# Optimization experiments

Hardware: AMD Instinct MI355X
Metric: run time of the kernel (lower is better)

The kernel has to match this reference:

```python
import math
import jax, jax.numpy as jnp
import numpy as np

H = 2048
T = 8192
NUM_LAYERS = 24
LAYER_ID = 6


def setup_inputs() -> dict:
    key = jax.random.key(0)
    ks = jax.random.split(key, 5)
    ratio_0_to_1 = LAYER_ID / (NUM_LAYERS - 1)
    ratio_1_to_almost_0 = 1.0 - LAYER_ID / NUM_LAYERS
    # parameter init exactly as in RwkvSelfAttention.__init__
    zigzag = 0.5 * (jnp.arange(1, H + 1) % 3 - 1)
    time_first = jnp.full((H,), math.log(0.3), jnp.float32) + zigzag.astype(jnp.float32)
    hh = jnp.arange(0, H, dtype=jnp.float32)
    time_decay = -5.0 + 8.0 * (hh / (H - 1)) ** (0.7 + 1.3 * ratio_0_to_1)
    xx = jnp.arange(H, dtype=jnp.float32) / H
    time_mix_key = jnp.power(xx, ratio_1_to_almost_0)
    time_mix_value = time_mix_key + 0.3 * ratio_0_to_1
    time_mix_receptance = jnp.power(xx, 0.5 * ratio_1_to_almost_0)
    scale = 1.0 / math.sqrt(H)
    return {
        "hidden": jax.random.normal(ks[0], (T, H), jnp.float32),
        "sx": jnp.zeros((H,), jnp.float32),
        "aa": jnp.zeros((H,), jnp.float32),
        "bb": jnp.zeros((H,), jnp.float32),
        "pp": jnp.full((H,), -1e30, jnp.float32),  # log-space -inf init
        "time_decay": time_decay,
        "time_first": time_first,
        "time_mix_key": time_mix_key,
        "time_mix_value": time_mix_value,
        "time_mix_receptance": time_mix_receptance,
        "Wk": jax.random.normal(ks[1], (H, H), jnp.float32) * scale,
        "Wv": jax.random.normal(ks[2], (H, H), jnp.float32) * scale,
        "Wr": jax.random.normal(ks[3], (H, H), jnp.float32) * scale,
        "Wo": jax.random.normal(ks[4], (H, H), jnp.float32) * scale,
    }


def reference(hidden, sx, aa, bb, pp, time_decay, time_first, time_mix_key,
              time_mix_value, time_mix_receptance, Wk, Wv, Wr, Wo):
    # token-shift mix: c_x[t] = hidden[t-1], c_x[0] = sx
    c_x = jnp.concatenate((sx[None, :], hidden[:-1, :]), axis=0)  # [T, H]
    key_x = hidden * time_mix_key + c_x * (1.0 - time_mix_key)
    value_x = hidden * time_mix_value + c_x * (1.0 - time_mix_value)
    receptance_x = hidden * time_mix_receptance + c_x * (1.0 - time_mix_receptance)

    r = jax.nn.sigmoid(receptance_x @ Wr)  # [T, H]
    k = key_x @ Wk                         # [T, H]
    v = value_x @ Wv                       # [T, H]

    w_decay = -jnp.exp(time_decay)  # [H]

    def step(state, kv):
        a, b, p = state
        kk, vv = kv
        # output with bonus (time_first)
        ww = time_first + kk
        q = jnp.maximum(p, ww)
        e1 = jnp.exp(p - q)
        e2 = jnp.exp(ww - q)
        out_t = (e1 * a + e2 * vv) / (e1 * b + e2)
        # state update with decay
        ww2 = w_decay + p
        q2 = jnp.maximum(ww2, kk)
        e1b = jnp.exp(ww2 - q2)
        e2b = jnp.exp(kk - q2)
        return (e1b * a + e2b * vv, e1b * b + e2b, q2), out_t

    (aa, bb, pp), wkv = jax.lax.scan(step, (aa, bb, pp), (k, v))  # wkv: [T, H]

    out = hidden + (r * wkv) @ Wo
    return out, hidden[-1, :], aa, bb, pp
```

## Files before the change

kernel.cpp:

```cpp
#include <hip/hip_runtime.h>
#include <stdint.h>

#define H 2048
#define T 8192
#define C_CH 128
#define L_CH 64

typedef unsigned short u16;
typedef unsigned int u32;

__device__ __forceinline__ float bf2f(u16 u) {
  return __uint_as_float(((u32)u) << 16);
}
__device__ __forceinline__ u16 f2bf(float f) {
  u32 u = __float_as_uint(f);
  u = u + 0x7FFFu + ((u >> 16) & 1u);
  return (u16)(u >> 16);
}
__device__ __forceinline__ bool in_is_bf16(const u32* ppw) {
  u32 w = ppw[0];
  return (w >> 16) == (w & 0xFFFFu);
}
__device__ __forceinline__ float ldin(const void* p, size_t i, bool bf) {
  return bf ? bf2f(((const u16*)p)[i]) : ((const float*)p)[i];
}
__device__ __forceinline__ void stout(void* p, size_t i, float v, bool bf) {
  if (bf) ((u16*)p)[i] = f2bf(v);
  else ((float*)p)[i] = v;
}

__global__ void mix3_kernel(const void* __restrict__ hidden,
                            const void* __restrict__ sx,
                            const void* __restrict__ tmk,
                            const void* __restrict__ tmv,
                            const void* __restrict__ tmr,
                            u16* __restrict__ outk, u16* __restrict__ outv,
                            u16* __restrict__ outr, const u32* __restrict__ ppw) {
  bool bf = in_is_bf16(ppw);
  int i = blockIdx.x * blockDim.x + threadIdx.x;
  int h = i & (H - 1);
  float hv = ldin(hidden, (size_t)i, bf);
  float cv = (i < H) ? ldin(sx, (size_t)h, bf) : ldin(hidden, (size_t)i - H, bf);
  float d = hv - cv;
  outk[i] = f2bf(cv + ldin(tmk, (size_t)h, bf) * d);
  outv[i] = f2bf(cv + ldin(tmv, (size_t)h, bf) * d);
  outr[i] = f2bf(cv + ldin(tmr, (size_t)h, bf) * d);
}

__global__ void transpose_kernel(const void* __restrict__ W, u16* __restrict__ Wt,
                                 const u32* __restrict__ ppw) {
  bool bf = in_is_bf16(ppw);
  __shared__ u16 tile[32][33];
  int bx = blockIdx.x * 32, by = blockIdx.y * 32;
  int tx = threadIdx.x, ty = threadIdx.y;
#pragma unroll
  for (int j = 0; j < 32; j += 8)
    tile[ty + j][tx] = f2bf(ldin(W, (size_t)(by + ty + j) * H + bx + tx, bf));
  __syncthreads();
#pragma unroll
  for (int j = 0; j < 32; j += 8)
    Wt[(size_t)(bx + ty + j) * H + by + tx] = tile[tx][ty + j];
}

typedef short bf16x8 __attribute__((ext_vector_type(8)));
typedef float f32x4 __attribute__((ext_vector_type(4)));

#define MODE_K 0
#define MODE_BF16 1
#define MODE_SIG 2
#define MODE_ADDH 3

__device__ __forceinline__ void gl_lds16(const short* g, short* l) {
  __builtin_amdgcn_global_load_lds((__attribute__((address_space(1))) void*)(g),
                                   (__attribute__((address_space(3))) void*)(l),
                                   16, 0, 0);
}

template <int MODE>
__global__ __launch_bounds__(256) void gemm_kernel(
    const u16* __restrict__ Au, const u16* __restrict__ Btu,
    void* __restrict__ C, const void* __restrict__ hid,
    const u32* __restrict__ ppw) {
  __shared__ short As[128 * 64];
  __shared__ short Bs[128 * 64];
  const short* A = (const short*)Au;
  const short* Bt = (const short*)Btu;

  const int bid = blockIdx.x;
  const int xcd = bid & 7;
  const int s = bid >> 3;
  const int mblk = (xcd << 3) | (s & 7);
  const int nblk = s >> 3;
  const int m0 = mblk * 128;
  const int n0 = nblk * 128;

  const int tid = threadIdx.x;
  const int lane = tid & 63;
  const int wid = tid >> 6;
  const int wm = wid >> 1;
  const int wn = wid & 1;
  const int lrow = lane & 15;
  const int quad = lane >> 4;

  const int srow = lane >> 2;
  const int scol = (lane & 3) * 8;
  const short* gA = A + (size_t)(m0 + wid * 32 + srow) * H + scol;
  const short* gB = Bt + (size_t)(n0 + wid * 32 + srow) * H + scol;
  short* lA = As + wid * 1024;
  short* lB = Bs + wid * 1024;

  f32x4 acc[4][4];
#pragma unroll
  for (int i = 0; i < 4; i++)
#pragma unroll
    for (int j = 0; j < 4; j++) acc[i][j] = (f32x4){0.f, 0.f, 0.f, 0.f};

  for (int k0 = 0; k0 < H; k0 += 64) {
    __syncthreads();
    gl_lds16(gA + k0, lA);
    gl_lds16(gA + k0 + 16 * H, lA + 512);
    gl_lds16(gB + k0, lB);
    gl_lds16(gB + k0 + 16 * H, lB + 512);
    gl_lds16(gA + k0 + 32, lA + 4096);
    gl_lds16(gA + k0 + 32 + 16 * H, lA + 4096 + 512);
    gl_lds16(gB + k0 + 32, lB + 4096);
    gl_lds16(gB + k0 + 32 + 16 * H, lB + 4096 + 512);
    __syncthreads();
#pragma unroll
    for (int sub = 0; sub < 2; sub++) {
      const short* as = As + sub * 4096;
      const short* bs = Bs + sub * 4096;
      bf16x8 af[4], bfr[4];
#pragma unroll
      for (int i = 0; i < 4; i++)
        af[i] = *(const bf16x8*)(as + (wm * 64 + i * 16 + lrow) * 32 + quad * 8);
#pragma unroll
      for (int j = 0; j < 4; j++)
        bfr[j] = *(const bf16x8*)(bs + (wn * 64 + j * 16 + lrow) * 32 + quad * 8);
#pragma unroll
      for (int i = 0; i < 4; i++)
#pragma unroll
        for (int j = 0; j < 4; j++)
          acc[i][j] = __builtin_amdgcn_mfma_f32_16x16x32_bf16(af[i], bfr[j], acc[i][j], 0, 0, 0);
    }
  }

  bool bf = (MODE == MODE_ADDH) ? in_is_bf16(ppw) : true;
#pragma unroll
  for (int i = 0; i < 4; i++) {
#pragma unroll
    for (int j = 0; j < 4; j++) {
#pragma unroll
      for (int reg = 0; reg < 4; reg++) {
        int row = m0 + wm * 64 + i * 16 + quad * 4 + reg;
        int col = n0 + wn * 64 + j * 16 + lrow;
        size_t idx = (size_t)row * H + col;
        float val = acc[i][j][reg];
        if (MODE == MODE_K || MODE == MODE_BF16) {
          ((u16*)C)[idx] = f2bf(val);
        } else if (MODE == MODE_SIG) {
          ((u16*)C)[idx] = f2bf(1.0f / (1.0f + __expf(-val)));
        } else {
          stout(C, idx, val + ldin(hid, idx, bf), bf);
        }
      }
    }
  }
}

__global__ __launch_bounds__(256) void wkv_local_kernel(
    const u16* __restrict__ kbuf, const u16* __restrict__ vbuf,
    const void* __restrict__ tdec,
    float* __restrict__ suma, float* __restrict__ sumb, float* __restrict__ sump,
    const u32* __restrict__ ppw) {
  bool bf = in_is_bf16(ppw);
  int h = blockIdx.x * 256 + threadIdx.x;
  int c = blockIdx.y;
  float w = -__expf(ldin(tdec, h, bf));
  float a = 0.f, b = 0.f, p = -1e30f;
  size_t base = (size_t)c * L_CH * H + h;
#pragma unroll 4
  for (int t = 0; t < L_CH; t++) {
    size_t idx = base + (size_t)t * H;
    float kk = bf2f(kbuf[idx]);
    float vv = bf2f(vbuf[idx]);
    float ww2 = w + p;
    float q2 = fmaxf(ww2, kk);
    float e1b = __expf(ww2 - q2), e2b = __expf(kk - q2);
    a = e1b * a + e2b * vv;
    b = e1b * b + e2b;
    p = q2;
  }
  suma[(size_t)c * H + h] = a;
  sumb[(size_t)c * H + h] = b;
  sump[(size_t)c * H + h] = p;
}

__global__ __launch_bounds__(256) void wkv_prefix_kernel(
    const float* __restrict__ suma, const float* __restrict__ sumb,
    const float* __restrict__ sump,
    const void* __restrict__ aa_in, const void* __restrict__ bb_in,
    const void* __restrict__ pp_in, const void* __restrict__ tdec,
    const void* __restrict__ hidden,
    float* __restrict__ sta, float* __restrict__ stb, float* __restrict__ stp,
    void* __restrict__ dout, const u32* __restrict__ ppw) {
  bool bf = in_is_bf16(ppw);
  int h = blockIdx.x * 256 + threadIdx.x;
  float a = ldin(aa_in, h, bf), b = ldin(bb_in, h, bf), p = ldin(pp_in, h, bf);
  float w = -__expf(ldin(tdec, h, bf));
  float wL = w * (float)L_CH;
  for (int c = 0; c < C_CH; c++) {
    size_t i = (size_t)c * H + h;
    sta[i] = a;
    stb[i] = b;
    stp[i] = p;
    float la = suma[i], lb = sumb[i], lp = sump[i];
    float pd = p + wL;
    float q = fmaxf(pd, lp);
    float e1 = __expf(pd - q), e2 = __expf(lp - q);
    a = e1 * a + e2 * la;
    b = e1 * b + e2 * lb;
    p = q;
  }
  size_t base = (size_t)T * H;
  stout(dout, base + h, ldin(hidden, (size_t)(T - 1) * H + h, bf), bf);
  stout(dout, base + H + h, a, bf);
  stout(dout, base + 2 * H + h, b, bf);
  stout(dout, base + 3 * H + h, p, bf);
}

__global__ __launch_bounds__(256) void wkv_out_kernel(
    const u16* __restrict__ kbuf, const u16* __restrict__ vbuf,
    const u16* __restrict__ rbuf,
    const float* __restrict__ sta, const float* __restrict__ stb,
    const float* __restrict__ stp,
    const void* __restrict__ tdec, const void* __restrict__ tfirst,
    u16* __restrict__ rw, const u32* __restrict__ ppw) {
  bool bf = in_is_bf16(ppw);
  int h = blockIdx.x * 256 + threadIdx.x;
  int c = blockIdx.y;
  size_t si = (size_t)c * H + h;
  float a = sta[si], b = stb[si], p = stp[si];
  float tf = ldin(tfirst, h, bf);
  float w = -__expf(ldin(tdec, h, bf));
  size_t base = (size_t)c * L_CH * H + h;
#pragma unroll 4
  for (int t = 0; t < L_CH; t++) {
    size_t idx = base + (size_t)t * H;
    float kk = bf2f(kbuf[idx]);
    float vv = bf2f(vbuf[idx]);
    float rr = bf2f(rbuf[idx]);
    float ww = tf + kk;
    float q = fmaxf(p, ww);
    float e1 = __expf(p - q), e2 = __expf(ww - q);
    float wkv = (e1 * a + e2 * vv) / (e1 * b + e2);
    rw[idx] = f2bf(rr * wkv);
    float ww2 = w + p;
    float q2 = fmaxf(ww2, kk);
    float e1b = __expf(ww2 - q2), e2b = __expf(kk - q2);
    a = e1b * a + e2b * vv;
    b = e1b * b + e2b;
    p = q2;
  }
}

extern "C" void kernel_launch(void* const* d_in, const int* in_sizes, int n_in,
                              void* d_out, int out_size, void* d_ws, size_t ws_size,
                              hipStream_t stream) {
  const void* hidden = d_in[0];
  const void* sx = d_in[1];
  const void* aa = d_in[2];
  const void* bb = d_in[3];
  const void* pp = d_in[4];
  const void* tdec = d_in[5];
  const void* tfirst = d_in[6];
  const void* tmk = d_in[7];
  const void* tmv = d_in[8];
  const void* tmr = d_in[9];
  const void* Wk = d_in[10];
  const void* Wv = d_in[11];
  const void* Wr = d_in[12];
  const void* Wo = d_in[13];
  const u32* ppw = (const u32*)d_in[4];

  char* ws = (char*)d_ws;
  const size_t TH2 = (size_t)T * H * 2;
  const size_t WT2 = (size_t)H * H * 2;
  u16* A1 = (u16*)ws;
  u16* A2 = (u16*)(ws + TH2);
  u16* A3 = (u16*)(ws + 2 * TH2);
  u16* B1 = (u16*)(ws + 3 * TH2);
  u16* Wt_buf = (u16*)(ws + 4 * TH2);
  float* suma = (float*)(ws + 4 * TH2 + WT2);
  float* sumb = suma + (size_t)C_CH * H;
  float* sump = sumb + (size_t)C_CH * H;
  float* sta = sump + (size_t)C_CH * H;
  float* stb = sta + (size_t)C_CH * H;
  float* stp = stb + (size_t)C_CH * H;

  dim3 mixG((T * H) / 256), mixB(256);
  dim3 trG(64, 64), trB(32, 8);
  dim3 gG(1024), gB(256);
  dim3 scG(H / 256, C_CH), scB(256);

  mix3_kernel<<<mixG, mixB, 0, stream>>>(hidden, sx, tmk, tmv, tmr,
                                         A1, A2, A3, ppw);
  transpose_kernel<<<trG, trB, 0, stream>>>(Wr, Wt_buf, ppw);
  gemm_kernel<MODE_SIG><<<gG, gB, 0, stream>>>(A3, Wt_buf, B1, nullptr, ppw);
  transpose_kernel<<<trG, trB, 0, stream>>>(Wk, Wt_buf, ppw);
  gemm_kernel<MODE_K><<<gG, gB, 0, stream>>>(A1, Wt_buf, A3, nullptr, ppw);
  transpose_kernel<<<trG, trB, 0, stream>>>(Wv, Wt_buf, ppw);
  gemm_kernel<MODE_BF16><<<gG, gB, 0, stream>>>(A2, Wt_buf, A1, nullptr, ppw);
  wkv_local_kernel<<<scG, scB, 0, stream>>>(A3, A1, tdec, suma, sumb, sump, ppw);
  wkv_prefix_kernel<<<dim3(H / 256), scB, 0, stream>>>(
      suma, sumb, sump, aa, bb, pp, tdec, hidden, sta, stb, stp, d_out, ppw);
  wkv_out_kernel<<<scG, scB, 0, stream>>>(A3, A1, B1, sta, stb, stp,
                                          tdec, tfirst, A2, ppw);
  transpose_kernel<<<trG, trB, 0, stream>>>(Wo, Wt_buf, ppw);
  gemm_kernel<MODE_ADDH><<<gG, gB, 0, stream>>>(A2, Wt_buf, d_out, hidden, ppw);
}
```

Baseline: 672.1 us.

## Double-buffer LDS tiles in bf16 GEMM to overlap global loads with MFMA

Splits the LDS tile into two 32-wide K buffers and stages the next half-tile with global_load_lds while MFMAs run on the current one. The aim is to hide global-memory latency that the old load-all, sync, compute loop left exposed. Total LDS use stays the same, but each barrier now covers half as much K. The overlap only happens if the compiler's vmcnt waits do not force the in-flight prefetch to finish before the current buffer is read.

```diff
diff --git a/kernel.cpp b/kernel.cpp
--- a/kernel.cpp
+++ b/kernel.cpp
@@ -81,8 +81,8 @@
     const u16* __restrict__ Au, const u16* __restrict__ Btu,
     void* __restrict__ C, const void* __restrict__ hid,
     const u32* __restrict__ ppw) {
-  __shared__ short As[128 * 64];
-  __shared__ short Bs[128 * 64];
+  __shared__ short As[2][128 * 32];
+  __shared__ short Bs[2][128 * 32];
   const short* A = (const short*)Au;
   const short* Bt = (const short*)Btu;
 
@@ -106,8 +106,7 @@
   const int scol = (lane & 3) * 8;
   const short* gA = A + (size_t)(m0 + wid * 32 + srow) * H + scol;
   const short* gB = Bt + (size_t)(n0 + wid * 32 + srow) * H + scol;
-  short* lA = As + wid * 1024;
-  short* lB = Bs + wid * 1024;
+  const int lofs = wid * 1024;
 
   f32x4 acc[4][4];
 #pragma unroll
@@ -115,35 +114,40 @@
 #pragma unroll
     for (int j = 0; j < 4; j++) acc[i][j] = (f32x4){0.f, 0.f, 0.f, 0.f};
 
+#define STAGE(kk, buf)                                   \
+  do {                                                   \
+    gl_lds16(gA + (kk), &As[buf][lofs]);                 \
+    gl_lds16(gA + (kk) + 16 * H, &As[buf][lofs + 512]);  \
+    gl_lds16(gB + (kk), &Bs[buf][lofs]);                 \
+    gl_lds16(gB + (kk) + 16 * H, &Bs[buf][lofs + 512]);  \
+  } while (0)
+
+#define COMPUTE(buf)                                                          \
+  do {                                                                        \
+    bf16x8 af[4], bfr[4];                                                     \
+    _Pragma("unroll") for (int i = 0; i < 4; i++)                             \
+        af[i] = *(const bf16x8*)(&As[buf][(wm * 64 + i * 16 + lrow) * 32 +    \
+                                          quad * 8]);                         \
+    _Pragma("unroll") for (int j = 0; j < 4; j++)                             \
+        bfr[j] = *(const bf16x8*)(&Bs[buf][(wn * 64 + j * 16 + lrow) * 32 +   \
+                                           quad * 8]);                        \
+    _Pragma("unroll") for (int i = 0; i < 4; i++)                             \
+        _Pragma("unroll") for (int j = 0; j < 4; j++) acc[i][j] =             \
+            __builtin_amdgcn_mfma_f32_16x16x32_bf16(af[i], bfr[j], acc[i][j], \
+                                                    0, 0, 0);                 \
+  } while (0)
+
+  STAGE(0, 0);
   for (int k0 = 0; k0 < H; k0 += 64) {
     __syncthreads();
-    gl_lds16(gA + k0, lA);
-    gl_lds16(gA + k0 + 16 * H, lA + 512);
-    gl_lds16(gB + k0, lB);
-    gl_lds16(gB + k0 + 16 * H, lB + 512);
-    gl_lds16(gA + k0 + 32, lA + 4096);
-    gl_lds16(gA + k0 + 32 + 16 * H, lA + 4096 + 512);
-    gl_lds16(gB + k0 + 32, lB + 4096);
-    gl_lds16(gB + k0 + 32 + 16 * H, lB + 4096 + 512);
+    STAGE(k0 + 32, 1);
+    COMPUTE(0);
     __syncthreads();
-#pragma unroll
-    for (int sub = 0; sub < 2; sub++) {
-      const short* as = As + sub * 4096;
-      const short* bs = Bs + sub * 4096;
-      bf16x8 af[4], bfr[4];
-#pragma unroll
-      for (int i = 0; i < 4; i++)
-        af[i] = *(const bf16x8*)(as + (wm * 64 + i * 16 + lrow) * 32 + quad * 8);
-#pragma unroll
-      for (int j = 0; j < 4; j++)
-        bfr[j] = *(const bf16x8*)(bs + (wn * 64 + j * 16 + lrow) * 32 + quad * 8);
-#pragma unroll
-      for (int i = 0; i < 4; i++)
-#pragma unroll
-        for (int j = 0; j < 4; j++)
-          acc[i][j] = __builtin_amdgcn_mfma_f32_16x16x32_bf16(af[i], bfr[j], acc[i][j], 0, 0, 0);
-    }
-  }
+    if (k0 + 64 < H) STAGE(k0 + 64, 0);
+    COMPUTE(1);
+  }
+#undef STAGE
+#undef COMPUTE
 
   bool bf = (MODE == MODE_ADDH) ? in_is_bf16(ppw) : true;
 #pragma unroll
```

After: 759.3 us. +13.0%, slower.
